# Kernel optimization log

Measured on AMD Instinct MI355X. Metric: run time of the kernel, lower is better.

## Reference

```python
import jax, jax.numpy as jnp
import numpy as np

# ---- geometry constants (from init_kwargs options) ----
VIEWS, NDET, NX, NY = 360, 736, 512, 512
DVOX, DDET = 0.7, 1.2858
DSO, DOD = 595.0, 490.6
DSD = DSO + DOD
STEP = 0.0174533
END_ANGLE = STEP * VIEWS  # ~2*pi
EXTENT = 1


def _compute_indices():
    """CPU port of PixelIndexCal_cuda (fanflat mode, extent=1).
    Returns flat int64 indices of shape [NX*NY*VIEWS] (pixel-major, view inner)."""
    sVx, sVy = DVOX * NX, DVOX * NY
    alphas = np.linspace(0.0, END_ANGLE, VIEWS, endpoint=False)
    indX, indY = np.meshgrid(np.arange(NX, dtype=np.float64),
                             np.arange(NY, dtype=np.float64), indexing='ij')
    idx_all = np.empty((NX * NY, VIEWS), dtype=np.int64)
    for a in range(VIEWS):
        alpha = -alphas[a]
        c, s = np.cos(alpha), np.sin(alpha)
        P0x = -(sVx / 2 - DVOX / 2)
        P0y = sVy / 2 - DVOX / 2
        rot = lambda px, py: (px * c + py * s, -px * s + py * c)
        Px_, Py_ = rot(P0x, P0y)
        Pxx, Pxy = rot(P0x + DVOX, P0y)
        Pyx, Pyy = rot(P0x, P0y - DVOX)
        Py_, Pxy, Pyy = Py_ / DDET, Pxy / DDET, Pyy / DDET
        dXx, dXy = Pxx - Px_, Pxy - Py_
        dYx, dYy = Pyx - Px_, Pyy - Py_
        # per-pixel rotated coords
        Pix = Px_ + indX * dXx + indY * dYx
        Piy = Py_ + indX * dXy + indY * dYy
        # fanflat: source at (DSO, 0); ray hits detector plane at x = DSO-DSD
        vectX = Pix - DSO
        t = -DSD / vectX
        det = Piy * t + NDET / 2.0
        det = np.clip(det, 1.0, NDET - 2.0)
        idx_all[:, a] = (det + NDET * a).astype(np.int64).ravel()
    return idx_all.reshape(-1)


def _conv(x, w, b):
    y = jax.lax.conv_general_dilated(x, w, (1, 1), 'SAME',
                                     dimension_numbers=('NCHW', 'OIHW', 'NCHW'))
    return y + b[None, :, None, None]


def setup_inputs() -> dict:
    key = jax.random.key(0)
    ks = jax.random.split(key, 16)
    lin_std = 1.0 / np.sqrt(NDET)
    conv_std = 1.0 / np.sqrt(64 * 9)
    inp = {
        'x': jax.random.normal(ks[0], (1, 1, VIEWS, NDET), jnp.float32),
        'indices': jnp.asarray(_compute_indices()),
        'w1': jax.random.normal(ks[1], (NDET, NDET), jnp.float32) * lin_std,
        'b1': jnp.zeros((NDET,), jnp.float32),
        'w2': jax.random.normal(ks[2], (NDET, NDET), jnp.float32) * lin_std,
        'b2': jnp.zeros((NDET,), jnp.float32),
        'conv_in_w': jax.random.normal(ks[3], (64, 1, 3, 3), jnp.float32) * (1.0 / 3.0),
        'conv_in_b': jnp.zeros((64,), jnp.float32),
        'blk_w1': jax.random.normal(ks[4], (11, 64, 64, 3, 3), jnp.float32) * conv_std,
        'blk_b1': jnp.zeros((11, 64), jnp.float32),
        'blk_w2': jax.random.normal(ks[5], (11, 64, 64, 3, 3), jnp.float32) * conv_std,
        'blk_b2': jnp.zeros((11, 64), jnp.float32),
        'conv_out_w': jax.random.normal(ks[6], (1, 64, 3, 3), jnp.float32) * conv_std,
        'conv_out_b': jnp.zeros((1,), jnp.float32),
    }
    return inp


def reference(x, indices, w1, b1, w2, b2, conv_in_w, conv_in_b,
              blk_w1, blk_b1, blk_w2, blk_b2, conv_out_w, conv_out_b):
    # convf: two per-detector-row Linear+ReLU over last dim (nDetecU)
    h = jax.nn.relu(x @ w1.T + b1)
    h = jax.nn.relu(h @ w2.T + b2)
    # BackProjNet (learn=False): gather + sum over views, scale, flip
    sino = h.reshape(-1, 1, VIEWS * NDET)
    g = sino[:, :, indices]                         # [B,1,NX*NY*VIEWS]
    g = g.reshape(-1, 1, NX * NY, VIEWS * EXTENT)
    img = g.sum(axis=3) * ((END_ANGLE - 0.0) / (2 * VIEWS * EXTENT))
    img = img.reshape(-1, 1, NX, NY)
    img = jnp.flip(img, axis=(2, 3))
    # rCNN refinement: conv(1->64)+ReLU, 11 residual blocks, conv(64->1)
    y = jax.nn.relu(_conv(img, conv_in_w, conv_in_b))
    for i in range(11):
        z = _conv(y, blk_w1[i], blk_b1[i])
        z = jax.nn.relu(z)
        z = _conv(z, blk_w2[i], blk_b2[i])
        y = jax.nn.relu(y + z)
    out = _conv(y, conv_out_w, conv_out_b)
    return out
```

## Files before the change

### kernel.cpp

```cpp
#include <hip/hip_runtime.h>

#define VIEWS 360
#define NDET 736
#define NX 512
#define NY 512
#define NPIX (NX * NY)

typedef unsigned short u16;
typedef __attribute__((ext_vector_type(8))) short bf16x8;
typedef __attribute__((ext_vector_type(4))) float f32x4;

__device__ __forceinline__ u16 f2bf(float f) {
  unsigned u = __float_as_uint(f);
  return (u16)((u + 0x7fffu + ((u >> 16) & 1u)) >> 16);
}
__device__ __forceinline__ float bf2f(u16 v) {
  return __uint_as_float(((unsigned)v) << 16);
}

__device__ __forceinline__ void gload_lds16(const void* g, void* l) {
  __builtin_amdgcn_global_load_lds(
      (const __attribute__((address_space(1))) void*)g,
      (__attribute__((address_space(3))) void*)l, 16, 0, 0);
}

__global__ __launch_bounds__(256) void linear_relu4_kernel(
    const float* __restrict__ in, const float* __restrict__ w,
    const float* __restrict__ b, float* __restrict__ out) {
  __shared__ __align__(16) float xin[4][NDET];
  const int v0 = blockIdx.x * 4;
  const int t = threadIdx.x;
  for (int k = t; k < 4 * (NDET / 4); k += 256) {
    const int row = k / (NDET / 4), c4 = k % (NDET / 4);
    ((float4*)xin[row])[c4] = ((const float4*)(in + (size_t)(v0 + row) * NDET))[c4];
  }
  __syncthreads();

  const bool has2 = (t < NDET - 512);
  const float4* w0 = (const float4*)(w + (size_t)t * NDET);
  const float4* w1 = (const float4*)(w + (size_t)(t + 256) * NDET);
  const float4* w2 = (const float4*)(w + (size_t)(has2 ? t + 512 : t) * NDET);

  float acc[3][4];
#pragma unroll
  for (int j = 0; j < 3; ++j)
#pragma unroll
    for (int v = 0; v < 4; ++v) acc[j][v] = 0.f;

#pragma unroll 2
  for (int k = 0; k < NDET / 4; ++k) {
    float4 xv0 = ((const float4*)xin[0])[k];
    float4 xv1 = ((const float4*)xin[1])[k];
    float4 xv2 = ((const float4*)xin[2])[k];
    float4 xv3 = ((const float4*)xin[3])[k];
    float4 wv;
    wv = w0[k];
    acc[0][0] = fmaf(xv0.x, wv.x, fmaf(xv0.y, wv.y, fmaf(xv0.z, wv.z, fmaf(xv0.w, wv.w, acc[0][0]))));
    acc[0][1] = fmaf(xv1.x, wv.x, fmaf(xv1.y, wv.y, fmaf(xv1.z, wv.z, fmaf(xv1.w, wv.w, acc[0][1]))));
    acc[0][2] = fmaf(xv2.x, wv.x, fmaf(xv2.y, wv.y, fmaf(xv2.z, wv.z, fmaf(xv2.w, wv.w, acc[0][2]))));
    acc[0][3] = fmaf(xv3.x, wv.x, fmaf(xv3.y, wv.y, fmaf(xv3.z, wv.z, fmaf(xv3.w, wv.w, acc[0][3]))));
    wv = w1[k];
    acc[1][0] = fmaf(xv0.x, wv.x, fmaf(xv0.y, wv.y, fmaf(xv0.z, wv.z, fmaf(xv0.w, wv.w, acc[1][0]))));
    acc[1][1] = fmaf(xv1.x, wv.x, fmaf(xv1.y, wv.y, fmaf(xv1.z, wv.z, fmaf(xv1.w, wv.w, acc[1][1]))));
    acc[1][2] = fmaf(xv2.x, wv.x, fmaf(xv2.y, wv.y, fmaf(xv2.z, wv.z, fmaf(xv2.w, wv.w, acc[1][2]))));
    acc[1][3] = fmaf(xv3.x, wv.x, fmaf(xv3.y, wv.y, fmaf(xv3.z, wv.z, fmaf(xv3.w, wv.w, acc[1][3]))));
    wv = w2[k];
    acc[2][0] = fmaf(xv0.x, wv.x, fmaf(xv0.y, wv.y, fmaf(xv0.z, wv.z, fmaf(xv0.w, wv.w, acc[2][0]))));
    acc[2][1] = fmaf(xv1.x, wv.x, fmaf(xv1.y, wv.y, fmaf(xv1.z, wv.z, fmaf(xv1.w, wv.w, acc[2][1]))));
    acc[2][2] = fmaf(xv2.x, wv.x, fmaf(xv2.y, wv.y, fmaf(xv2.z, wv.z, fmaf(xv2.w, wv.w, acc[2][2]))));
    acc[2][3] = fmaf(xv3.x, wv.x, fmaf(xv3.y, wv.y, fmaf(xv3.z, wv.z, fmaf(xv3.w, wv.w, acc[2][3]))));
  }

  const float b0 = b[t], b1 = b[t + 256];
  const float b2v = has2 ? b[t + 512] : 0.f;
#pragma unroll
  for (int v = 0; v < 4; ++v) {
    float* o = out + (size_t)(v0 + v) * NDET;
    o[t] = fmaxf(acc[0][v] + b0, 0.f);
    o[t + 256] = fmaxf(acc[1][v] + b1, 0.f);
    if (has2) o[t + 512] = fmaxf(acc[2][v] + b2v, 0.f);
  }
}

__global__ __launch_bounds__(256) void backproj_kernel(
    const float* __restrict__ sino, const int* __restrict__ idx,
    float* __restrict__ img) {
  __shared__ int lidx[256 * 77];
  const int t = threadIdx.x;
  const int p_base = blockIdx.x * 256;

  float a0 = 0.f, a1 = 0.f, a2 = 0.f, a3 = 0.f;

#pragma unroll 1
  for (int c = 0; c < 5; ++c) {
    if (c) __syncthreads();
#pragma unroll
    for (int k = 0; k < 18; ++k) {
      const int f = k * 256 + t;
      const int row = f / 18, col4 = f % 18;
      int4 v = *(const int4*)&idx[(size_t)(p_base + row) * VIEWS + c * 72 +
                                  col4 * 4];
      int* dst = &lidx[row * 77 + col4 * 4];
      dst[0] = v.x; dst[1] = v.y; dst[2] = v.z; dst[3] = v.w;
    }
    __syncthreads();
    const int* myrow = &lidx[t * 77];
#pragma unroll
    for (int j = 0; j < 72; j += 4) {
      a0 += sino[myrow[j + 0]];
      a1 += sino[myrow[j + 1]];
      a2 += sino[myrow[j + 2]];
      a3 += sino[myrow[j + 3]];
    }
  }

  const int p = p_base + t;
  const int ix = p >> 9, iy = p & 511;
  img[(NX - 1 - ix) * NY + (NY - 1 - iy)] =
      ((a0 + a1) + (a2 + a3)) * 0.00872665f;
}

__device__ __forceinline__ void load9(const float* __restrict__ base, int gx,
                                      int gy, float v[9]) {
  const bool xm = gx > 0, xp = gx < NX - 1, ym = gy > 0, yp = gy < NY - 1;
  const float* c = base + gy * NX + gx;
  v[0] = (ym && xm) ? c[-NX - 1] : 0.f;
  v[1] = (ym)       ? c[-NX]     : 0.f;
  v[2] = (ym && xp) ? c[-NX + 1] : 0.f;
  v[3] = (xm)       ? c[-1]      : 0.f;
  v[4] =               c[0];
  v[5] = (xp)       ? c[1]       : 0.f;
  v[6] = (yp && xm) ? c[NX - 1]  : 0.f;
  v[7] = (yp)       ? c[NX]      : 0.f;
  v[8] = (yp && xp) ? c[NX + 1]  : 0.f;
}

__device__ __forceinline__ float dot9(float a, const float v[9],
                                      const float* __restrict__ w) {
  a = fmaf(v[0], w[0], a);
  a = fmaf(v[1], w[1], a);
  a = fmaf(v[2], w[2], a);
  a = fmaf(v[3], w[3], a);
  a = fmaf(v[4], w[4], a);
  a = fmaf(v[5], w[5], a);
  a = fmaf(v[6], w[6], a);
  a = fmaf(v[7], w[7], a);
  a = fmaf(v[8], w[8], a);
  return a;
}

__global__ __launch_bounds__(256) void conv_in_kernel(
    const float* __restrict__ in, const float* __restrict__ w,
    const float* __restrict__ b, float* __restrict__ outf,
    u16* __restrict__ outb) {
  const int p = blockIdx.x * 256 + threadIdx.x;
  const int gx = p & (NX - 1), gy = p >> 9;
  float v[9];
  load9(in, gx, gy, v);
  float4* of = (float4*)(outf + (size_t)p * 64);
  uint4* ob = (uint4*)(outb + (size_t)p * 64);
#pragma unroll
  for (int oq = 0; oq < 8; ++oq) {
    float f[8];
#pragma unroll
    for (int c = 0; c < 8; ++c)
      f[c] = fmaxf(dot9(b[oq * 8 + c], v, w + (oq * 8 + c) * 9), 0.f);
    of[oq * 2 + 0] = (float4){f[0], f[1], f[2], f[3]};
    of[oq * 2 + 1] = (float4){f[4], f[5], f[6], f[7]};
    uint4 pk;
    pk.x = (unsigned)f2bf(f[0]) | ((unsigned)f2bf(f[1]) << 16);
    pk.y = (unsigned)f2bf(f[2]) | ((unsigned)f2bf(f[3]) << 16);
    pk.z = (unsigned)f2bf(f[4]) | ((unsigned)f2bf(f[5]) << 16);
    pk.w = (unsigned)f2bf(f[6]) | ((unsigned)f2bf(f[7]) << 16);
    ob[oq] = pk;
  }
}

__global__ __launch_bounds__(256) void prep_weights_kernel(
    const float* __restrict__ bw1, const float* __restrict__ bw2,
    u16* __restrict__ wR) {
  const int g = blockIdx.x * 256 + threadIdx.x;
  if (g >= 22 * 36864) return;
  if (g < 32) wR[22 * 36864 + g] = 0;
  const int li = g / 36864, r1 = g % 36864;
  const int s = r1 / 2048, r2 = r1 % 2048;
  const int lane = r2 / 32, r3 = r2 % 32;
  const int mf = r3 / 8, j = r3 % 8;
  const int kb = s / 9, tap = s % 9;
  const int kg = lane >> 4, n = lane & 15;
  const int oc = mf * 16 + n;
  const int ic = kb * 32 + kg * 8 + j;
  const float* src = (li < 11) ? bw1 + li * 36864 : bw2 + (li - 11) * 36864;
  wR[g] = f2bf(src[(oc * 64 + ic) * 9 + tap]);
}

template <int ADDRES, int DUALOUT>
__global__ __launch_bounds__(256, 4) void conv64_mfma(
    const u16* __restrict__ in_, const u16* __restrict__ wA,
    const float* __restrict__ bias, const float* __restrict__ res,
    u16* __restrict__ outb, float* __restrict__ outf,
    const u16* __restrict__ zpad) {
  __shared__ __align__(16) u16 lds[6 * 66 * 32];
  const int xb = (blockIdx.x & 7) * 64;
  const int yb = (int)(blockIdx.x >> 3) * 4;
  const int tid = threadIdx.x;
  const int wv = tid >> 6;
  const int lane = tid & 63;
  const int n = lane & 15;
  const int kg = lane >> 4;

  f32x4 acc[4][4];
#pragma unroll
  for (int i = 0; i < 4; ++i)
#pragma unroll
    for (int j = 0; j < 4; ++j) acc[i][j] = (f32x4){0.f, 0.f, 0.f, 0.f};

#pragma unroll 1
  for (int kb = 0; kb < 2; ++kb) {
    if (kb) __syncthreads();
#pragma unroll
    for (int it = 0; it < 7; ++it) {
      const int g = it * 256 + tid;
      if (it < 6 || g < 1584) {
        const int j = g & 3;
        const int xr = g >> 2;
        const int x66 = xr % 66;
        const int r = xr / 66;
        const int y = yb - 1 + r;
        const int x = xb - 1 + x66;
        const int icq = j ^ ((x66 >> 1) & 3);
        const u16* src = zpad;
        if ((unsigned)y < 512u && (unsigned)x < 512u)
          src = in_ + ((size_t)((y << 9) + x)) * 64 + kb * 32 + icq * 8;
        gload_lds16(src, &lds[(size_t)(g & ~63) * 8]);
      }
    }
    __syncthreads();

#pragma unroll 3
    for (int tap = 0; tap < 9; ++tap) {
      const int s = kb * 9 + tap;
      bf16x8 av[4];
#pragma unroll
      for (int mf = 0; mf < 4; ++mf)
        av[mf] = *(const bf16x8*)&wA[((size_t)s * 64 + lane) * 32 + mf * 8];

      const int r = wv + tap / 3;
      const int dxp1 = tap % 3;

      bf16x8 bfr[4];
#pragma unroll
      for (int nf = 0; nf < 4; ++nf) {
        const int xi = dxp1 + nf * 16 + n;
        const int slot = kg ^ ((xi >> 1) & 3);
        bfr[nf] = *(const bf16x8*)&lds[((r * 66 + xi) * 4 + slot) * 8];
      }
#pragma unroll
      for (int mf = 0; mf < 4; ++mf)
#pragma unroll
        for (int nf = 0; nf < 4; ++nf)
          acc[mf][nf] = __builtin_amdgcn_mfma_f32_16x16x32_bf16(
              av[mf], bfr[nf], acc[mf][nf], 0, 0, 0);
    }
  }

  const int y = yb + wv;
#pragma unroll
  for (int mf = 0; mf < 4; ++mf) {
    const float4 bv = *(const float4*)&bias[mf * 16 + kg * 4];
#pragma unroll
    for (int nf = 0; nf < 4; ++nf) {
      const int x = xb + nf * 16 + n;
      const size_t base = ((size_t)((y << 9) + x)) * 64 + mf * 16 + kg * 4;
      float v0 = acc[mf][nf][0] + bv.x;
      float v1 = acc[mf][nf][1] + bv.y;
      float v2 = acc[mf][nf][2] + bv.z;
      float v3 = acc[mf][nf][3] + bv.w;
      if (ADDRES) {
        float4 rr = *(const float4*)&res[base];
        v0 += rr.x; v1 += rr.y; v2 += rr.z; v3 += rr.w;
      }
      v0 = fmaxf(v0, 0.f); v1 = fmaxf(v1, 0.f);
      v2 = fmaxf(v2, 0.f); v3 = fmaxf(v3, 0.f);
      uint2 pk;
      pk.x = (unsigned)f2bf(v0) | ((unsigned)f2bf(v1) << 16);
      pk.y = (unsigned)f2bf(v2) | ((unsigned)f2bf(v3) << 16);
      *(uint2*)&outb[base] = pk;
      if (DUALOUT) {
        *(float4*)&outf[base] = (float4){v0, v1, v2, v3};
      }
    }
  }
}

__global__ __launch_bounds__(256) void conv_out_kernel(
    const float* __restrict__ in, const float* __restrict__ w,
    const float* __restrict__ b, float* __restrict__ out) {
  const int p = blockIdx.x * 256 + threadIdx.x;
  const int gx = p & (NX - 1), gy = p >> 9;
  float a = b[0];
#pragma unroll
  for (int ty = 0; ty < 3; ++ty) {
#pragma unroll
    for (int tx = 0; tx < 3; ++tx) {
      const int yy = gy + ty - 1, xx = gx + tx - 1;
      if ((unsigned)yy < 512u && (unsigned)xx < 512u) {
        const float4* q = (const float4*)(in + ((size_t)((yy << 9) + xx)) * 64);
        const int tap = ty * 3 + tx;
#pragma unroll
        for (int i = 0; i < 16; ++i) {
          float4 d = q[i];
          a = fmaf(d.x, w[(i * 4 + 0) * 9 + tap], a);
          a = fmaf(d.y, w[(i * 4 + 1) * 9 + tap], a);
          a = fmaf(d.z, w[(i * 4 + 2) * 9 + tap], a);
          a = fmaf(d.w, w[(i * 4 + 3) * 9 + tap], a);
        }
      }
    }
  }
  out[p] = a;
}

extern "C" void kernel_launch(void* const* d_in, const int* in_sizes, int n_in,
                              void* d_out, int out_size, void* d_ws,
                              size_t ws_size, hipStream_t stream) {
  const float* x      = (const float*)d_in[0];
  const int*   indices= (const int*)d_in[1];
  const float* w1     = (const float*)d_in[2];
  const float* b1     = (const float*)d_in[3];
  const float* w2     = (const float*)d_in[4];
  const float* b2     = (const float*)d_in[5];
  const float* cin_w  = (const float*)d_in[6];
  const float* cin_b  = (const float*)d_in[7];
  const float* bw1    = (const float*)d_in[8];
  const float* bb1    = (const float*)d_in[9];
  const float* bw2    = (const float*)d_in[10];
  const float* bb2    = (const float*)d_in[11];
  const float* cout_w = (const float*)d_in[12];
  const float* cout_b = (const float*)d_in[13];

  float* ws   = (float*)d_ws;
  float* h1   = ws;
  float* h2   = h1 + VIEWS * NDET;
  float* img  = h2 + VIEWS * NDET;
  float* yf   = img + NPIX;
  u16*  ybf   = (u16*)(yf + (size_t)64 * NPIX);
  u16*  zb    = ybf + (size_t)64 * NPIX;
  u16*  wAll  = zb + (size_t)64 * NPIX;
  u16*  zpad  = wAll + 22 * 36864;

  prep_weights_kernel<<<(22 * 36864 + 255) / 256, 256, 0, stream>>>(bw1, bw2,
                                                                    wAll);
  linear_relu4_kernel<<<VIEWS / 4, 256, 0, stream>>>(x, w1, b1, h1);
  linear_relu4_kernel<<<VIEWS / 4, 256, 0, stream>>>(h1, w2, b2, h2);
  backproj_kernel<<<NPIX / 256, 256, 0, stream>>>(h2, indices, img);
  conv_in_kernel<<<NPIX / 256, 256, 0, stream>>>(img, cin_w, cin_b, yf, ybf);

  for (int i = 0; i < 11; ++i) {
    conv64_mfma<0, 0><<<1024, 256, 0, stream>>>(
        ybf, wAll + i * 36864, bb1 + i * 64, nullptr, zb, nullptr, zpad);
    conv64_mfma<1, 1><<<1024, 256, 0, stream>>>(
        zb, wAll + (11 + i) * 36864, bb2 + i * 64, yf, ybf, yf, zpad);
  }
  conv_out_kernel<<<NPIX / 256, 256, 0, stream>>>(yf, cout_w, cout_b,
                                                  (float*)d_out);
}
```

Before: 1.927 ms.

## Register-staged double load in conv64, fuse linear layers, reorder weight layout

The conv64 MFMA kernel drops the direct global-to-LDS loads. It stages each half of the input tile through registers, issuing the second half's global loads before computing on the first half so that memory latency overlaps the MFMAs. The two Linear+ReLU kernels are fused into one kernel that keeps the intermediate in shared memory, saving a launch and a global round-trip. The weight layout is reordered so each mf fragment is read contiguously per lane. Register staging raises register pressure under the 4-waves launch bound, which could lower occupancy or cause spills.

```diff
diff --git a/kernel.cpp b/kernel.cpp
--- a/kernel.cpp
+++ b/kernel.cpp
@@ -10,75 +10,89 @@
 typedef __attribute__((ext_vector_type(8))) short bf16x8;
 typedef __attribute__((ext_vector_type(4))) float f32x4;
 
+#define BAR_LDS() asm volatile("s_waitcnt lgkmcnt(0)\n\ts_barrier" ::: "memory")
+
 __device__ __forceinline__ u16 f2bf(float f) {
   unsigned u = __float_as_uint(f);
   return (u16)((u + 0x7fffu + ((u >> 16) & 1u)) >> 16);
 }
-__device__ __forceinline__ float bf2f(u16 v) {
-  return __uint_as_float(((unsigned)v) << 16);
-}
-
-__device__ __forceinline__ void gload_lds16(const void* g, void* l) {
-  __builtin_amdgcn_global_load_lds(
-      (const __attribute__((address_space(1))) void*)g,
-      (__attribute__((address_space(3))) void*)l, 16, 0, 0);
-}
-
-__global__ __launch_bounds__(256) void linear_relu4_kernel(
-    const float* __restrict__ in, const float* __restrict__ w,
-    const float* __restrict__ b, float* __restrict__ out) {
+
+__global__ __launch_bounds__(256) void linear2_kernel(
+    const float* __restrict__ x, const float* __restrict__ w1,
+    const float* __restrict__ b1, const float* __restrict__ w2,
+    const float* __restrict__ b2, float* __restrict__ out) {
   __shared__ __align__(16) float xin[4][NDET];
+  __shared__ __align__(16) float h1s[4][NDET];
   const int v0 = blockIdx.x * 4;
   const int t = threadIdx.x;
   for (int k = t; k < 4 * (NDET / 4); k += 256) {
     const int row = k / (NDET / 4), c4 = k % (NDET / 4);
-    ((float4*)xin[row])[c4] = ((const float4*)(in + (size_t)(v0 + row) * NDET))[c4];
+    ((float4*)xin[row])[c4] =
+        ((const float4*)(x + (size_t)(v0 + row) * NDET))[c4];
   }
   __syncthreads();
 
   const bool has2 = (t < NDET - 512);
-  const float4* w0 = (const float4*)(w + (size_t)t * NDET);
-  const float4* w1 = (const float4*)(w + (size_t)(t + 256) * NDET);
-  const float4* w2 = (const float4*)(w + (size_t)(has2 ? t + 512 : t) * NDET);
-
-  float acc[3][4];
-#pragma unroll
-  for (int j = 0; j < 3; ++j)
-#pragma unroll
-    for (int v = 0; v < 4; ++v) acc[j][v] = 0.f;
+
+#pragma unroll 1
+  for (int L = 0; L < 2; ++L) {
+    const float* w = L ? w2 : w1;
+    const float* b = L ? b2 : b1;
+    const float(*src)[NDET] = L ? h1s : xin;
+
+    const float4* w0 = (const float4*)(w + (size_t)t * NDET);
+    const float4* w1p = (const float4*)(w + (size_t)(t + 256) * NDET);
+    const float4* w2p = (const float4*)(w + (size_t)(has2 ? t + 512 : t) * NDET);
+
+    float acc[3][4];
+#pragma unroll
+    for (int j = 0; j < 3; ++j)
+#pragma unroll
+      for (int v = 0; v < 4; ++v) acc[j][v] = 0.f;
 
 #pragma unroll 2
-  for (int k = 0; k < NDET / 4; ++k) {
-    float4 xv0 = ((const float4*)xin[0])[k];
-    float4 xv1 = ((const float4*)xin[1])[k];
-    float4 xv2 = ((const float4*)xin[2])[k];
-    float4 xv3 = ((const float4*)xin[3])[k];
-    float4 wv;
-    wv = w0[k];
-    acc[0][0] = fmaf(xv0.x, wv.x, fmaf(xv0.y, wv.y, fmaf(xv0.z, wv.z, fmaf(xv0.w, wv.w, acc[0][0]))));
-    acc[0][1] = fmaf(xv1.x, wv.x, fmaf(xv1.y, wv.y, fmaf(xv1.z, wv.z, fmaf(xv1.w, wv.w, acc[0][1]))));
-    acc[0][2] = fmaf(xv2.x, wv.x, fmaf(xv2.y, wv.y, fmaf(xv2.z, wv.z, fmaf(xv2.w, wv.w, acc[0][2]))));
-    acc[0][3] = fmaf(xv3.x, wv.x, fmaf(xv3.y, wv.y, fmaf(xv3.z, wv.z, fmaf(xv3.w, wv.w, acc[0][3]))));
-    wv = w1[k];
-    acc[1][0] = fmaf(xv0.x, wv.x, fmaf(xv0.y, wv.y, fmaf(xv0.z, wv.z, fmaf(xv0.w, wv.w, acc[1][0]))));
-    acc[1][1] = fmaf(xv1.x, wv.x, fmaf(xv1.y, wv.y, fmaf(xv1.z, wv.z, fmaf(xv1.w, wv.w, acc[1][1]))));
-    acc[1][2] = fmaf(xv2.x, wv.x, fmaf(xv2.y, wv.y, fmaf(xv2.z, wv.z, fmaf(xv2.w, wv.w, acc[1][2]))));
-    acc[1][3] = fmaf(xv3.x, wv.x, fmaf(xv3.y, wv.y, fmaf(xv3.z, wv.z, fmaf(xv3.w, wv.w, acc[1][3]))));
-    wv = w2[k];
-    acc[2][0] = fmaf(xv0.x, wv.x, fmaf(xv0.y, wv.y, fmaf(xv0.z, wv.z, fmaf(xv0.w, wv.w, acc[2][0]))));
-    acc[2][1] = fmaf(xv1.x, wv.x, fmaf(xv1.y, wv.y, fmaf(xv1.z, wv.z, fmaf(xv1.w, wv.w, acc[2][1]))));
-    acc[2][2] = fmaf(xv2.x, wv.x, fmaf(xv2.y, wv.y, fmaf(xv2.z, wv.z, fmaf(xv2.w, wv.w, acc[2][2]))));
-    acc[2][3] = fmaf(xv3.x, wv.x, fmaf(xv3.y, wv.y, fmaf(xv3.z, wv.z, fmaf(xv3.w, wv.w, acc[2][3]))));
-  }
-
-  const float b0 = b[t], b1 = b[t + 256];
-  const float b2v = has2 ? b[t + 512] : 0.f;
-#pragma unroll
-  for (int v = 0; v < 4; ++v) {
-    float* o = out + (size_t)(v0 + v) * NDET;
-    o[t] = fmaxf(acc[0][v] + b0, 0.f);
-    o[t + 256] = fmaxf(acc[1][v] + b1, 0.f);
-    if (has2) o[t + 512] = fmaxf(acc[2][v] + b2v, 0.f);
+    for (int k = 0; k < NDET / 4; ++k) {
+      float4 xv0 = ((const float4*)src[0])[k];
+      float4 xv1 = ((const float4*)src[1])[k];
+      float4 xv2 = ((const float4*)src[2])[k];
+      float4 xv3 = ((const float4*)src[3])[k];
+      float4 wv;
+      wv = w0[k];
+      acc[0][0] = fmaf(xv0.x, wv.x, fmaf(xv0.y, wv.y, fmaf(xv0.z, wv.z, fmaf(xv0.w, wv.w, acc[0][0]))));
+      acc[0][1] = fmaf(xv1.x, wv.x, fmaf(xv1.y, wv.y, fmaf(xv1.z, wv.z, fmaf(xv1.w, wv.w, acc[0][1]))));
+      acc[0][2] = fmaf(xv2.x, wv.x, fmaf(xv2.y, wv.y, fmaf(xv2.z, wv.z, fmaf(xv2.w, wv.w, acc[0][2]))));
+      acc[0][3] = fmaf(xv3.x, wv.x, fmaf(xv3.y, wv.y, fmaf(xv3.z, wv.z, fmaf(xv3.w, wv.w, acc[0][3]))));
+      wv = w1p[k];
+      acc[1][0] = fmaf(xv0.x, wv.x, fmaf(xv0.y, wv.y, fmaf(xv0.z, wv.z, fmaf(xv0.w, wv.w, acc[1][0]))));
+      acc[1][1] = fmaf(xv1.x, wv.x, fmaf(xv1.y, wv.y, fmaf(xv1.z, wv.z, fmaf(xv1.w, wv.w, acc[1][1]))));
+      acc[1][2] = fmaf(xv2.x, wv.x, fmaf(xv2.y, wv.y, fmaf(xv2.z, wv.z, fmaf(xv2.w, wv.w, acc[1][2]))));
+      acc[1][3] = fmaf(xv3.x, wv.x, fmaf(xv3.y, wv.y, fmaf(xv3.z, wv.z, fmaf(xv3.w, wv.w, acc[1][3]))));
+      wv = w2p[k];
+      acc[2][0] = fmaf(xv0.x, wv.x, fmaf(xv0.y, wv.y, fmaf(xv0.z, wv.z, fmaf(xv0.w, wv.w, acc[2][0]))));
+      acc[2][1] = fmaf(xv1.x, wv.x, fmaf(xv1.y, wv.y, fmaf(xv1.z, wv.z, fmaf(xv1.w, wv.w, acc[2][1]))));
+      acc[2][2] = fmaf(xv2.x, wv.x, fmaf(xv2.y, wv.y, fmaf(xv2.z, wv.z, fmaf(xv2.w, wv.w, acc[2][2]))));
+      acc[2][3] = fmaf(xv3.x, wv.x, fmaf(xv3.y, wv.y, fmaf(xv3.z, wv.z, fmaf(xv3.w, wv.w, acc[2][3]))));
+    }
+
+    const float b0 = b[t], b1v = b[t + 256];
+    const float b2v = has2 ? b[t + 512] : 0.f;
+    if (L == 0) {
+#pragma unroll
+      for (int v = 0; v < 4; ++v) {
+        h1s[v][t] = fmaxf(acc[0][v] + b0, 0.f);
+        h1s[v][t + 256] = fmaxf(acc[1][v] + b1v, 0.f);
+        if (has2) h1s[v][t + 512] = fmaxf(acc[2][v] + b2v, 0.f);
+      }
+      __syncthreads();
+    } else {
+#pragma unroll
+      for (int v = 0; v < 4; ++v) {
+        float* o = out + (size_t)(v0 + v) * NDET;
+        o[t] = fmaxf(acc[0][v] + b0, 0.f);
+        o[t + 256] = fmaxf(acc[1][v] + b1v, 0.f);
+        if (has2) o[t + 512] = fmaxf(acc[2][v] + b2v, 0.f);
+      }
+    }
   }
 }
 
@@ -181,11 +195,10 @@
     u16* __restrict__ wR) {
   const int g = blockIdx.x * 256 + threadIdx.x;
   if (g >= 22 * 36864) return;
-  if (g < 32) wR[22 * 36864 + g] = 0;
   const int li = g / 36864, r1 = g % 36864;
   const int s = r1 / 2048, r2 = r1 % 2048;
-  const int lane = r2 / 32, r3 = r2 % 32;
-  const int mf = r3 / 8, j = r3 % 8;
+  const int mf = r2 / 512, r3 = r2 % 512;
+  const int lane = r3 / 8, j = r3 % 8;
   const int kb = s / 9, tap = s % 9;
   const int kg = lane >> 4, n = lane & 15;
   const int oc = mf * 16 + n;
@@ -194,12 +207,82 @@
   wR[g] = f2bf(src[(oc * 64 + ic) * 9 + tap]);
 }
 
-template <int ADDRES, int DUALOUT>
+__device__ __forceinline__ void stage_load(const u16* __restrict__ in_, int xb,
+                                           int yb, int tid, int kb,
+                                           uint4 p[7]) {
+#pragma unroll
+  for (int it = 0; it < 7; ++it) {
+    const int g = it * 256 + tid;
+    uint4 d = {0u, 0u, 0u, 0u};
+    if (g < 1584) {
+      const int icq = g & 3;
+      const int xr = g >> 2;
+      const int x66 = xr % 66;
+      const int r = xr / 66;
+      const int y = yb - 1 + r;
+      const int x = xb - 1 + x66;
+      if ((unsigned)y < 512u && (unsigned)x < 512u) {
+        const size_t gi = ((size_t)((y << 9) + x)) * 64 + kb * 32 + icq * 8;
+        d = *(const uint4*)&in_[gi];
+      }
+    }
+    p[it] = d;
+  }
+}
+
+__device__ __forceinline__ void stage_write(u16* lds, int tid,
+                                            const uint4 p[7]) {
+#pragma unroll
+  for (int it = 0; it < 7; ++it) {
+    const int g = it * 256 + tid;
+    if (g < 1584) {
+      const int icq = g & 3;
+      const int xr = g >> 2;
+      const int x66 = xr % 66;
+      const int slot = icq ^ ((x66 >> 1) & 3);
+      *(uint4*)&lds[(xr * 4 + slot) * 8] = p[it];
+    }
+  }
+}
+
+__device__ __forceinline__ void compute_half(const u16* lds,
+                                             const u16* __restrict__ wA,
+                                             int kb, int wv, int lane,
+                                             f32x4 acc[4][4]) {
+  const int n = lane & 15;
+  const int kg = lane >> 4;
+#pragma unroll 3
+  for (int tap = 0; tap < 9; ++tap) {
+    const int s = kb * 9 + tap;
+    bf16x8 av[4];
+#pragma unroll
+    for (int mf = 0; mf < 4; ++mf)
+      av[mf] = *(const bf16x8*)&wA[(size_t)s * 2048 + mf * 512 + lane * 8];
+
+    const int r = wv + tap / 3;
+    const int dxp1 = tap % 3;
+
+    bf16x8 bfr[4];
+#pragma unroll
+    for (int nf = 0; nf < 4; ++nf) {
+      const int xi = dxp1 + nf * 16 + n;
+      const int slot = kg ^ ((xi >> 1) & 3);
+      bfr[nf] = *(const bf16x8*)&lds[((r * 66 + xi) * 4 + slot) * 8];
+    }
+#pragma unroll
+    for (int mf = 0; mf < 4; ++mf)
+#pragma unroll
+      for (int nf = 0; nf < 4; ++nf)
+        acc[mf][nf] = __builtin_amdgcn_mfma_f32_16x16x32_bf16(
+            av[mf], bfr[nf], acc[mf][nf], 0, 0, 0);
+  }
+}
+
+template <int SUB>
 __global__ __launch_bounds__(256, 4) void conv64_mfma(
     const u16* __restrict__ in_, const u16* __restrict__ wA,
     const float* __restrict__ bias, const float* __restrict__ res,
-    u16* __restrict__ outb, float* __restrict__ outf,
-    const u16* __restrict__ zpad) {
+    void* __restrict__ out_, u16* __restrict__ outs) {
   __shared__ __align__(16) u16 lds[6 * 66 * 32];
   const int xb = (blockIdx.x & 7) * 64;
   const int yb = (int)(blockIdx.x >> 3) * 4;
@@ -215,54 +298,16 @@
 #pragma unroll
     for (int j = 0; j < 4; ++j) acc[i][j] = (f32x4){0.f, 0.f, 0.f, 0.f};
 
-#pragma unroll 1
-  for (int kb = 0; kb < 2; ++kb) {
-    if (kb) __syncthreads();
-#pragma unroll
-    for (int it = 0; it < 7; ++it) {
-      const int g = it * 256 + tid;
-      if (it < 6 || g < 1584) {
-        const int j = g & 3;
-        const int xr = g >> 2;
-        const int x66 = xr % 66;
-        const int r = xr / 66;
-        const int y = yb - 1 + r;
-        const int x = xb - 1 + x66;
-        const int icq = j ^ ((x66 >> 1) & 3);
-        const u16* src = zpad;
-        if ((unsigned)y < 512u && (unsigned)x < 512u)
-          src = in_ + ((size_t)((y << 9) + x)) * 64 + kb * 32 + icq * 8;
-        gload_lds16(src, &lds[(size_t)(g & ~63) * 8]);
-      }
-    }
-    __syncthreads();
-
-#pragma unroll 3
-    for (int tap = 0; tap < 9; ++tap) {
-      const int s = kb * 9 + tap;
-      bf16x8 av[4];
-#pragma unroll
-      for (int mf = 0; mf < 4; ++mf)
-        av[mf] = *(const bf16x8*)&wA[((size_t)s * 64 + lane) * 32 + mf * 8];
-
-      const int r = wv + tap / 3;
-      const int dxp1 = tap % 3;
-
-      bf16x8 bfr[4];
-#pragma unroll
-      for (int nf = 0; nf < 4; ++nf) {
-        const int xi = dxp1 + nf * 16 + n;
-        const int slot = kg ^ ((xi >> 1) & 3);
-        bfr[nf] = *(const bf16x8*)&lds[((r * 66 + xi) * 4 + slot) * 8];
-      }
-#pragma unroll
-      for (int mf = 0; mf < 4; ++mf)
-#pragma unroll
-        for (int nf = 0; nf < 4; ++nf)
-          acc[mf][nf] = __builtin_amdgcn_mfma_f32_16x16x32_bf16(
-              av[mf], bfr[nf], acc[mf][nf], 0, 0, 0);
-    }
-  }
+  uint4 p[7];
+  stage_load(in_, xb, yb, tid, 0, p);
+  stage_write(lds, tid, p);
+  stage_load(in_, xb, yb, tid, 1, p);
+  BAR_LDS();
+  compute_half(lds, wA, 0, wv, lane, acc);
+  BAR_LDS();
+  stage_write(lds, tid, p);
+  BAR_LDS();
+  compute_half(lds, wA, 1, wv, lane, acc);
 
   const int y = yb + wv;
 #pragma unroll
@@ -276,18 +321,23 @@
       float v1 = acc[mf][nf][1] + bv.y;
       float v2 = acc[mf][nf][2] + bv.z;
       float v3 = acc[mf][nf][3] + bv.w;
-      if (ADDRES) {
+      if (SUB) {
         float4 rr = *(const float4*)&res[base];
         v0 += rr.x; v1 += rr.y; v2 += rr.z; v3 += rr.w;
-      }
-      v0 = fmaxf(v0, 0.f); v1 = fmaxf(v1, 0.f);
-      v2 = fmaxf(v2, 0.f); v3 = fmaxf(v3, 0.f);
-      uint2 pk;
-      pk.x = (unsigned)f2bf(v0) | ((unsigned)f2bf(v1) << 16);
-      pk.y = (unsigned)f2bf(v2) | ((unsigned)f2bf(v3) << 16);
-      *(uint2*)&outb[base] = pk;
-      if (DUALOUT) {
-        *(float4*)&outf[base] = (float4){v0, v1, v2, v3};
+        v0 = fmaxf(v0, 0.f); v1 = fmaxf(v1, 0.f);
+        v2 = fmaxf(v2, 0.f); v3 = fmaxf(v3, 0.f);
+        *(float4*)&((float*)out_)[base] = (float4){v0, v1, v2, v3};
+        uint2 pk;
+        pk.x = (unsigned)f2bf(v0) | ((unsigned)f2bf(v1) << 16);
+        pk.y = (unsigned)f2bf(v2) | ((unsigned)f2bf(v3) << 16);
+        *(uint2*)&outs[base] = pk;
+      } else {
+        v0 = fmaxf(v0, 0.f); v1 = fmaxf(v1, 0.f);
+        v2 = fmaxf(v2, 0.f); v3 = fmaxf(v3, 0.f);
+        uint2 pk;
+        pk.x = (unsigned)f2bf(v0) | ((unsigned)f2bf(v1) << 16);
+        pk.y = (unsigned)f2bf(v2) | ((unsigned)f2bf(v3) << 16);
+        *(uint2*)&((u16*)out_)[base] = pk;
       }
     }
   }
@@ -340,27 +390,24 @@
   const float* cout_b = (const float*)d_in[13];
 
   float* ws   = (float*)d_ws;
-  float* h1   = ws;
-  float* h2   = h1 + VIEWS * NDET;
+  float* h2   = ws;
   float* img  = h2 + VIEWS * NDET;
   float* yf   = img + NPIX;
   u16*  ybf   = (u16*)(yf + (size_t)64 * NPIX);
   u16*  zb    = ybf + (size_t)64 * NPIX;
   u16*  wAll  = zb + (size_t)64 * NPIX;
-  u16*  zpad  = wAll + 22 * 36864;
 
   prep_weights_kernel<<<(22 * 36864 + 255) / 256, 256, 0, stream>>>(bw1, bw2,
                                                                     wAll);
-  linear_relu4_kernel<<<VIEWS / 4, 256, 0, stream>>>(x, w1, b1, h1);
-  linear_relu4_kernel<<<VIEWS / 4, 256, 0, stream>>>(h1, w2, b2, h2);
+  linear2_kernel<<<VIEWS / 4, 256, 0, stream>>>(x, w1, b1, w2, b2, h2);
   backproj_kernel<<<NPIX / 256, 256, 0, stream>>>(h2, indices, img);
   conv_in_kernel<<<NPIX / 256, 256, 0, stream>>>(img, cin_w, cin_b, yf, ybf);
 
   for (int i = 0; i < 11; ++i) {
-    conv64_mfma<0, 0><<<1024, 256, 0, stream>>>(
-        ybf, wAll + i * 36864, bb1 + i * 64, nullptr, zb, nullptr, zpad);
-    conv64_mfma<1, 1><<<1024, 256, 0, stream>>>(
-        zb, wAll + (11 + i) * 36864, bb2 + i * 64, yf, ybf, yf, zpad);
+    conv64_mfma<0><<<1024, 256, 0, stream>>>(
+        ybf, wAll + i * 36864, bb1 + i * 64, nullptr, zb, nullptr);
+    conv64_mfma<1><<<1024, 256, 0, stream>>>(
+        zb, wAll + (11 + i) * 36864, bb2 + i * 64, yf, yf, ybf);
   }
   conv_out_kernel<<<NPIX / 256, 256, 0, stream>>>(yf, cout_w, cout_b,
                                                   (float*)d_out);
```

New measurement: 1.955 ms. No clear change (+1.5%).
